# Optimization experiments

Measured on AMD Instinct MI355X. Metric: run time of the kernel, lower is better.

The kernel has to match this reference:

```python
import jax, jax.numpy as jnp
import numpy as np
from jax import lax

B, T, F, H, V, L = 64, 80, 4096, 512, 32000, 31


def _rn(k, shape, scale=0.05):
    return jax.random.normal(k, shape, dtype=jnp.float32) * scale


def setup_inputs() -> dict:
    key = jax.random.key(0)
    ks = jax.random.split(key, 16)
    emb = _rn(ks[0], (V, H)).at[0].set(0.0)  # padding_idx=0 row zeroed
    return dict(
        video_features=jax.random.normal(ks[1], (B, T, F), jnp.float32),
        captions=jax.random.randint(ks[2], (B, L), 0, V, jnp.int64),
        emb=emb,
        enc_Wih=_rn(ks[3], (4 * H, F)), enc_Whh=_rn(ks[4], (4 * H, H)),
        enc_bih=_rn(ks[5], (4 * H,)), enc_bhh=_rn(ks[6], (4 * H,)),
        attn_W=_rn(ks[7], (H, 2 * H)), attn_b=_rn(ks[8], (H,)),
        v_w=_rn(ks[9], (H,)),
        dec_Wih=_rn(ks[10], (4 * H, 2 * H)), dec_Whh=_rn(ks[11], (4 * H, H)),
        dec_bih=_rn(ks[12], (4 * H,)), dec_bhh=_rn(ks[13], (4 * H,)),
        fc_W=_rn(ks[14], (V, H)), fc_b=_rn(ks[15], (V,)),
    )


def _lstm_step(x, h, c, Wih, Whh, bih, bhh):
    # PyTorch gate order: i, f, g, o
    g = x @ Wih.T + bih + h @ Whh.T + bhh
    i, f, gg, o = jnp.split(g, 4, axis=-1)
    c = jax.nn.sigmoid(f) * c + jax.nn.sigmoid(i) * jnp.tanh(gg)
    h = jax.nn.sigmoid(o) * jnp.tanh(c)
    return h, c


def reference(video_features, captions, emb, enc_Wih, enc_Whh, enc_bih, enc_bhh,
              attn_W, attn_b, v_w, dec_Wih, dec_Whh, dec_bih, dec_bhh, fc_W, fc_b):
    b = video_features.shape[0]
    h_dim = enc_Whh.shape[1]
    h0 = jnp.zeros((b, h_dim), video_features.dtype)
    c0 = jnp.zeros((b, h_dim), video_features.dtype)

    # ---- encoder LSTM over time ----
    def enc_step(carry, x):
        h, c = carry
        h, c = _lstm_step(x, h, c, enc_Wih, enc_Whh, enc_bih, enc_bhh)
        return (h, c), h

    (h, c), enc_out = lax.scan(enc_step, (h0, c0), video_features.transpose(1, 0, 2))
    enc_out = enc_out.transpose(1, 0, 2)  # [B, T, H]

    # ---- attentive decoder, teacher forcing always on ----
    tokens = captions[:, :-1].T  # [L-1, B]

    def dec_step(carry, tok):
        h, c = carry
        e = emb[tok]  # [B, H]
        # Bahdanau attention: v . tanh(W [h; enc_out])
        hrep = jnp.broadcast_to(h[:, None, :], enc_out.shape)
        energy = jnp.tanh(jnp.concatenate([hrep, enc_out], axis=2) @ attn_W.T + attn_b)
        scores = energy @ v_w  # [B, T]
        w = jax.nn.softmax(scores, axis=1)
        ctx = jnp.einsum('bt,bth->bh', w, enc_out)
        x = jnp.concatenate([e, ctx], axis=1)  # [B, 2H]
        h, c = _lstm_step(x, h, c, dec_Wih, dec_Whh, dec_bih, dec_bhh)
        logits = h @ fc_W.T + fc_b  # [B, V]
        return (h, c), logits

    _, outs = lax.scan(dec_step, (h, c), tokens)
    return outs.transpose(1, 0, 2)  # [B, L-1, V]
```

## Files before the change

kernel.cpp:

```cpp
#include <hip/hip_runtime.h>


#define DEV __device__ __forceinline__

typedef __attribute__((ext_vector_type(4))) float f32x4;
typedef __attribute__((ext_vector_type(8))) short bf16x8;
typedef _Float16 half2_t __attribute__((ext_vector_type(2)));

static constexpr int B_ = 64, T_ = 80, H_ = 512, L_ = 31, NDEC = 30;

DEV unsigned short f2bf(float f) {
  unsigned u = __builtin_bit_cast(unsigned, f);
  u += 0x7FFF + ((u >> 16) & 1);
  return (unsigned short)(u >> 16);
}
DEV float bf2f(unsigned short s) {
  unsigned u = (unsigned)s << 16;
  return __builtin_bit_cast(float, u);
}
DEV unsigned short f2h(float x) { return __builtin_bit_cast(unsigned short, (_Float16)x); }
DEV float h2f(unsigned short h) { return (float)__builtin_bit_cast(_Float16, h); }
DEV unsigned f2h2(float lo, float hi) { return (unsigned)f2h(lo) | ((unsigned)f2h(hi) << 16); }
DEV float fdot2(unsigned x, unsigned w, float acc) {
  return __builtin_amdgcn_fdot2(__builtin_bit_cast(half2_t, x),
                                __builtin_bit_cast(half2_t, w), acc, false);
}
DEV float4 acc8(float4 a, uint4 hv, uint4 w0, uint4 w1, uint4 w2, uint4 w3) {
  a.x = fdot2(hv.x, w0.x, a.x); a.y = fdot2(hv.x, w0.y, a.y);
  a.z = fdot2(hv.x, w0.z, a.z); a.w = fdot2(hv.x, w0.w, a.w);
  a.x = fdot2(hv.y, w1.x, a.x); a.y = fdot2(hv.y, w1.y, a.y);
  a.z = fdot2(hv.y, w1.z, a.z); a.w = fdot2(hv.y, w1.w, a.w);
  a.x = fdot2(hv.z, w2.x, a.x); a.y = fdot2(hv.z, w2.y, a.y);
  a.z = fdot2(hv.z, w2.z, a.z); a.w = fdot2(hv.z, w2.w, a.w);
  a.x = fdot2(hv.w, w3.x, a.x); a.y = fdot2(hv.w, w3.y, a.y);
  a.z = fdot2(hv.w, w3.z, a.z); a.w = fdot2(hv.w, w3.w, a.w);
  return a;
}
DEV float accS(float s, uint4 hv, uint4 w) {
  s = fdot2(hv.x, w.x, s); s = fdot2(hv.y, w.y, s);
  s = fdot2(hv.z, w.z, s); s = fdot2(hv.w, w.w, s);
  return s;
}
DEV float sigmoidf(float x) { return 1.f / (1.f + __expf(-x)); }
DEV float tanh_fast(float x) { float e = __expf(2.f * x); return (e - 1.f) / (e + 1.f); }

DEV void astf(float* p, float v) { __hip_atomic_store(p, v, __ATOMIC_RELAXED, __HIP_MEMORY_SCOPE_AGENT); }
DEV void astu(unsigned* p, unsigned v) { __hip_atomic_store(p, v, __ATOMIC_RELAXED, __HIP_MEMORY_SCOPE_AGENT); }
DEV void asti(int* p, int v) { __hip_atomic_store(p, v, __ATOMIC_RELAXED, __HIP_MEMORY_SCOPE_AGENT); }
DEV float aldf(const float* p) { return __hip_atomic_load((float*)p, __ATOMIC_RELAXED, __HIP_MEMORY_SCOPE_AGENT); }
DEV unsigned aldu(const unsigned* p) { return __hip_atomic_load((unsigned*)p, __ATOMIC_RELAXED, __HIP_MEMORY_SCOPE_AGENT); }
DEV int aldi(const int* p) { return __hip_atomic_load((int*)p, __ATOMIC_RELAXED, __HIP_MEMORY_SCOPE_AGENT); }

DEV void tsync8(int* tf, int m, int ph) {
  __syncthreads();
  if (threadIdx.x == 0) asti(tf + m * 16, ph);
  if (threadIdx.x < 8)
    while (aldi(tf + (int)threadIdx.x * 16) < ph) __builtin_amdgcn_s_sleep(1);
  __syncthreads();
}

__global__ __launch_bounds__(256) void k_cvt(const float* __restrict__ in,
                                             unsigned short* __restrict__ out, long n4) {
  long i = (long)blockIdx.x * 256 + threadIdx.x;
  long stride = (long)gridDim.x * 256;
  for (; i < n4; i += stride) {
    float4 v = reinterpret_cast<const float4*>(in)[i];
    ushort4 o;
    o.x = f2bf(v.x); o.y = f2bf(v.y); o.z = f2bf(v.z); o.w = f2bf(v.w);
    reinterpret_cast<ushort4*>(out)[i] = o;
  }
}

__global__ void k_detect_i64(const int* __restrict__ cap, int* __restrict__ flag) {
  __shared__ int s;
  if (threadIdx.x == 0) s = 0;
  __syncthreads();
  int acc = 0;
  for (int i = threadIdx.x; i < (B_ * L_) / 2; i += 256) acc |= cap[2 * i + 1];
  if (acc) atomicOr(&s, 1);
  __syncthreads();
  if (threadIdx.x == 0) flag[0] = (s == 0) ? 1 : 0;
}

__global__ __launch_bounds__(256) void k_gather_emb(const float* __restrict__ emb,
                                                    const int* __restrict__ cap,
                                                    const int* __restrict__ flag,
                                                    unsigned short* __restrict__ aemb) {
  int r = blockIdx.x;
  int l = r >> 6, b = r & 63;
  int ci = b * L_ + l;
  int tok = flag[0] ? cap[2 * ci] : cap[ci];
  const float* src = emb + (size_t)tok * H_;
  unsigned short* dst = aemb + (size_t)r * H_;
  for (int c = threadIdx.x; c < H_; c += 256) dst[c] = f2bf(src[c]);
}

__global__ __launch_bounds__(256) void k_pack_enc(const float* __restrict__ whh,
                                                  uint4* __restrict__ wpe) {
  int idx = blockIdx.x * 256 + threadIdx.x;
  int k2 = idx >> 9, j = idx & 511;
  float2 r0 = *(const float2*)(whh + (size_t)(j) * 512 + 2 * k2);
  float2 r1 = *(const float2*)(whh + (size_t)(512 + j) * 512 + 2 * k2);
  float2 r2 = *(const float2*)(whh + (size_t)(1024 + j) * 512 + 2 * k2);
  float2 r3 = *(const float2*)(whh + (size_t)(1536 + j) * 512 + 2 * k2);
  wpe[idx] = make_uint4(f2h2(r0.x, r0.y), f2h2(r1.x, r1.y), f2h2(r2.x, r2.y), f2h2(r3.x, r3.y));
}

__global__ __launch_bounds__(256) void k_pack_dec(const float* __restrict__ dwih,
                                                  const float* __restrict__ dwhh,
                                                  uint4* __restrict__ wpd) {
  int idx = blockIdx.x * 256 + threadIdx.x;
  int k2 = idx >> 9, j = idx & 511;
  float2 r[4];
  if (k2 < 256) {
#pragma unroll
    for (int g = 0; g < 4; ++g)
      r[g] = *(const float2*)(dwih + (size_t)(g * 512 + j) * 1024 + 512 + 2 * k2);
  } else {
#pragma unroll
    for (int g = 0; g < 4; ++g)
      r[g] = *(const float2*)(dwhh + (size_t)(g * 512 + j) * 512 + 2 * (k2 - 256));
  }
  wpd[idx] = make_uint4(f2h2(r[0].x, r[0].y), f2h2(r[1].x, r[1].y),
                        f2h2(r[2].x, r[2].y), f2h2(r[3].x, r[3].y));
}

__global__ __launch_bounds__(256) void k_pack_attn2(const float* __restrict__ attnw,
                                                    uint4* __restrict__ wat2) {
  int idx = blockIdx.x * 256 + threadIdx.x;
  int k8 = idx >> 9, u = idx & 511;
  const float* p = attnw + (size_t)u * 1024 + 8 * k8;
  wat2[idx] = make_uint4(f2h2(p[0], p[1]), f2h2(p[2], p[3]),
                         f2h2(p[4], p[5]), f2h2(p[6], p[7]));
}

template <int OUT_MODE>
__global__ __launch_bounds__(256) void k_gemm(const unsigned short* __restrict__ A, int lda,
                                              const unsigned short* __restrict__ Bm, int ldb,
                                              float* __restrict__ C, int N, int K,
                                              const float* __restrict__ bias0,
                                              const float* __restrict__ bias1) {
  __shared__ __align__(16) unsigned short As[128 * 40];
  __shared__ __align__(16) unsigned short Bs[128 * 40];
  const int tid = threadIdx.x;
  const int m0 = blockIdx.y * 128, n0 = blockIdx.x * 128;
  const int wave = tid >> 6, lane = tid & 63;
  const int wm = wave >> 1, wn = wave & 1;
  const int lr = lane & 15, lk = lane >> 4;

  f32x4 acc[4][4];
#pragma unroll
  for (int m = 0; m < 4; ++m)
#pragma unroll
    for (int n = 0; n < 4; ++n) acc[m][n] = (f32x4){0.f, 0.f, 0.f, 0.f};

  const int c0 = tid, c1 = tid + 256;
  const int ar0 = c0 >> 2, as0 = c0 & 3;
  const int ar1 = c1 >> 2, as1 = c1 & 3;
  const unsigned short* pa0 = A + (size_t)(m0 + ar0) * lda + as0 * 8;
  const unsigned short* pa1 = A + (size_t)(m0 + ar1) * lda + as1 * 8;
  const unsigned short* pb0 = Bm + (size_t)(n0 + ar0) * ldb + as0 * 8;
  const unsigned short* pb1 = Bm + (size_t)(n0 + ar1) * ldb + as1 * 8;

  uint4 va0 = *(const uint4*)(pa0);
  uint4 va1 = *(const uint4*)(pa1);
  uint4 vb0 = *(const uint4*)(pb0);
  uint4 vb1 = *(const uint4*)(pb1);

  for (int k0 = 0; k0 < K; k0 += 32) {
    *(uint4*)(As + ar0 * 40 + as0 * 8) = va0;
    *(uint4*)(As + ar1 * 40 + as1 * 8) = va1;
    *(uint4*)(Bs + ar0 * 40 + as0 * 8) = vb0;
    *(uint4*)(Bs + ar1 * 40 + as1 * 8) = vb1;
    __syncthreads();
    if (k0 + 32 < K) {
      va0 = *(const uint4*)(pa0 + k0 + 32);
      va1 = *(const uint4*)(pa1 + k0 + 32);
      vb0 = *(const uint4*)(pb0 + k0 + 32);
      vb1 = *(const uint4*)(pb1 + k0 + 32);
    }
    bf16x8 af[4], bfr[4];
#pragma unroll
    for (int m = 0; m < 4; ++m)
      af[m] = *(const bf16x8*)(As + (wm * 64 + m * 16 + lr) * 40 + lk * 8);
#pragma unroll
    for (int n = 0; n < 4; ++n)
      bfr[n] = *(const bf16x8*)(Bs + (wn * 64 + n * 16 + lr) * 40 + lk * 8);
#pragma unroll
    for (int m = 0; m < 4; ++m)
#pragma unroll
      for (int n = 0; n < 4; ++n)
        acc[m][n] = __builtin_amdgcn_mfma_f32_16x16x32_bf16(af[m], bfr[n], acc[m][n], 0, 0, 0);
    __syncthreads();
  }
#pragma unroll
  for (int m = 0; m < 4; ++m) {
#pragma unroll
    for (int n = 0; n < 4; ++n) {
      const int col = n0 + wn * 64 + n * 16 + lr;
      float bv = (bias0 ? bias0[col] : 0.f) + (bias1 ? bias1[col] : 0.f);
#pragma unroll
      for (int j = 0; j < 4; ++j) {
        const int row = m0 + wm * 64 + m * 16 + lk * 4 + j;
        float v = acc[m][n][j] + bv;
        if (OUT_MODE == 0) {
          C[(size_t)row * N + col] = v;
        } else if (OUT_MODE == 1) {
          int l = row >> 6, b = row & 63;
          C[((size_t)b * NDEC + l) * (size_t)N + col] = v;
        } else {
          C[((size_t)row * 512 + (col & 511)) * 4 + (col >> 9)] = v;
        }
      }
    }
  }
}

__global__ __launch_bounds__(1024) void k_enc6(const float4* __restrict__ xg4,
                                               const uint4* __restrict__ wpe,
                                               float* __restrict__ encf,
                                               unsigned short* __restrict__ encbf,
                                               float* __restrict__ cfin,
                                               unsigned* __restrict__ h16E,
                                               int* __restrict__ flagsE) {
  __shared__ __align__(16) unsigned short h16[2][512];
  __shared__ __align__(16) float psumG[2][16][4][64];
  __shared__ __align__(16) float gsum[2][4][64];
  __shared__ unsigned short hnew[2][64];
  __shared__ __align__(16) uint4 wcache[96 * 64];
  const int bid = blockIdx.x, team = bid >> 3, m = bid & 7, tid = threadIdx.x;
  const int J0 = m * 64;
  int* tf = flagsE + team * 128;
  for (int i = tid; i < 96 * 64; i += 1024)
    wcache[i] = wpe[((i >> 6) << 9) | (J0 + (i & 63))];
  if (tid < 512) { h16[0][tid] = 0; h16[1][tid] = 0; }
  float c = 0.f;
  __syncthreads();
  const int j64 = tid & 63, ks = tid >> 6;
  const int j = J0 + j64;
  const uint4* hp0 = (const uint4*)h16[0];
  const uint4* hp1 = (const uint4*)h16[1];
  for (int t = 0; t < T_; ++t) {
    float4 a0 = {0.f, 0.f, 0.f, 0.f}, a1 = a0;
    if (ks < 6) {
#pragma unroll
      for (int ii = 0; ii < 4; ++ii) {
        const int k8 = ks * 4 + ii;
        uint4 h0 = hp0[k8], h1 = hp1[k8];
        uint4 w0 = wcache[((k8 * 4 + 0) << 6) | j64];
        uint4 w1 = wcache[((k8 * 4 + 1) << 6) | j64];
        uint4 w2 = wcache[((k8 * 4 + 2) << 6) | j64];
        uint4 w3 = wcache[((k8 * 4 + 3) << 6) | j64];
        a0 = acc8(a0, h0, w0, w1, w2, w3);
        a1 = acc8(a1, h1, w0, w1, w2, w3);
      }
    } else {
#pragma unroll 2
      for (int ii = 0; ii < 4; ++ii) {
        const int k8 = ks * 4 + ii;
        uint4 h0 = hp0[k8], h1 = hp1[k8];
        uint4 w0 = wpe[((k8 * 4 + 0) << 9) | j];
        uint4 w1 = wpe[((k8 * 4 + 1) << 9) | j];
        uint4 w2 = wpe[((k8 * 4 + 2) << 9) | j];
        uint4 w3 = wpe[((k8 * 4 + 3) << 9) | j];
        a0 = acc8(a0, h0, w0, w1, w2, w3);
        a1 = acc8(a1, h1, w0, w1, w2, w3);
      }
    }
    psumG[0][ks][0][j64] = a0.x; psumG[0][ks][1][j64] = a0.y;
    psumG[0][ks][2][j64] = a0.z; psumG[0][ks][3][j64] = a0.w;
    psumG[1][ks][0][j64] = a1.x; psumG[1][ks][1][j64] = a1.y;
    psumG[1][ks][2][j64] = a1.z; psumG[1][ks][3][j64] = a1.w;
    __syncthreads();
    if (tid < 512) {
      const int b2 = tid >> 8, g = (tid >> 6) & 3, jj = tid & 63;
      float s = 0.f;
#pragma unroll
      for (int q = 0; q < 16; ++q) s += psumG[b2][q][g][jj];
      gsum[b2][g][jj] = s;
    }
    __syncthreads();
    if (tid < 128) {
      const int b2 = tid >> 6, jj = tid & 63;
      const int b = team * 2 + b2;
      float4 xa = xg4[((size_t)b * T_ + t) * 512 + J0 + jj];
      float g0 = xa.x + gsum[b2][0][jj];
      float g1 = xa.y + gsum[b2][1][jj];
      float g2 = xa.z + gsum[b2][2][jj];
      float g3 = xa.w + gsum[b2][3][jj];
      c = sigmoidf(g1) * c + sigmoidf(g0) * tanh_fast(g2);
      float h = sigmoidf(g3) * tanh_fast(c);
      size_t o = ((size_t)b * T_ + t) * 512 + J0 + jj;
      encf[o] = h;
      encbf[o] = f2bf(h);
      hnew[b2][jj] = f2h(h);
      if (t == T_ - 1) cfin[(size_t)b * 512 + J0 + jj] = c;
    }
    __syncthreads();
    const int p = t & 1;
    if (tid < 64) {
      const int b2 = tid >> 5, pp = tid & 31;
      const int b = team * 2 + b2;
      astu(h16E + (size_t)p * 64 * 256 + b * 256 + (J0 >> 1) + pp,
           f2h2(h2f(hnew[b2][2 * pp]), h2f(hnew[b2][2 * pp + 1])));
    }
    tsync8(tf, m, t + 1);
    if (t < T_ - 1) {
      if (tid < 512) {
        const int b2 = tid >> 8, pp = tid & 255;
        const int b = team * 2 + b2;
        ((unsigned*)h16[b2])[pp] = aldu(h16E + (size_t)p * 64 * 256 + b * 256 + pp);
      }
      __syncthreads();
    }
  }
}

__global__ __launch_bounds__(1024) void k_dec8(const uint4* __restrict__ wpd,
                                               const uint4* __restrict__ wat2,
                                               const float* __restrict__ vw,
                                               const float4* __restrict__ eg4,
                                               const float* __restrict__ encpart,
                                               const unsigned short* __restrict__ encbf,
                                               const float* __restrict__ encf,
                                               const float* __restrict__ cfin,
                                               unsigned short* __restrict__ hsbf,
                                               float* __restrict__ scpart,
                                               unsigned* __restrict__ ctxsl,
                                               unsigned* __restrict__ h16D,
                                               int* __restrict__ flagsD) {
  __shared__ __align__(16) unsigned short xv16[2][1024];
  __shared__ float vsmO[64];
  __shared__ float hwOwn[2][64];
  __shared__ float sc2[2][80], wts2[2][80];
  __shared__ __align__(16) float psumW[2][16][64];
  __shared__ __align__(16) float psumG[2][16][4][64];
  __shared__ __align__(16) float gsum[2][4][64];
  __shared__ __align__(16) float ctxp[2][8][64];
  __shared__ unsigned short hnew[2][64];
  const int bid = blockIdx.x, team = bid >> 3, m = bid & 7, tid = threadIdx.x;
  const int J0 = m * 64;
  int* tf = flagsD + team * 128;
  {
    const int b2 = tid >> 9, jj = tid & 511;
    xv16[b2][512 + jj] = f2h(encf[((size_t)(team * 2 + b2) * T_ + T_ - 1) * 512 + jj]);
  }
  if (tid < 64) vsmO[tid] = vw[J0 + tid];
  float c = 0.f;
  if (tid < 128) c = cfin[(size_t)(team * 2 + (tid >> 6)) * 512 + J0 + (tid & 63)];
  __syncthreads();
  const int j64 = tid & 63, ks = tid >> 6;
  const int j = J0 + j64;
  const uint4* xp0 = (const uint4*)xv16[0];
  const uint4* xp1 = (const uint4*)xv16[1];

  for (int l = 0; l < NDEC; ++l) {
    {
      float4 a0 = {0.f, 0.f, 0.f, 0.f}, a1 = a0;
      float s0 = 0.f, s1 = 0.f;
#pragma unroll 2
      for (int ii = 0; ii < 4; ++ii) {
        const int ka = ks * 4 + ii;
        const int kg = 64 + ka;
        uint4 hx0 = xp0[kg], hx1 = xp1[kg];
        uint4 w0 = wpd[((kg * 4 + 0) << 9) | j];
        uint4 w1 = wpd[((kg * 4 + 1) << 9) | j];
        uint4 w2 = wpd[((kg * 4 + 2) << 9) | j];
        uint4 w3 = wpd[((kg * 4 + 3) << 9) | j];
        a0 = acc8(a0, hx0, w0, w1, w2, w3);
        a1 = acc8(a1, hx1, w0, w1, w2, w3);
        uint4 wa = wat2[(ka << 9) | j];
        s0 = accS(s0, hx0, wa);
        s1 = accS(s1, hx1, wa);
      }
      psumG[0][ks][0][j64] = a0.x; psumG[0][ks][1][j64] = a0.y;
      psumG[0][ks][2][j64] = a0.z; psumG[0][ks][3][j64] = a0.w;
      psumG[1][ks][0][j64] = a1.x; psumG[1][ks][1][j64] = a1.y;
      psumG[1][ks][2][j64] = a1.z; psumG[1][ks][3][j64] = a1.w;
      psumW[0][ks][j64] = s0;
      psumW[1][ks][j64] = s1;
    }
    __syncthreads();
    if (tid < 128) {
      const int b2 = tid >> 6, jj = tid & 63;
      float s = 0.f;
#pragma unroll
      for (int q = 0; q < 16; ++q) s += psumW[b2][q][jj];
      hwOwn[b2][jj] = s;
    }
    __syncthreads();
    {
      const int wv = tid >> 6, ln = tid & 63;
      const int b2 = wv & 1, b = team * 2 + b2;
      for (int t = wv >> 1; t < T_; t += 8) {
        float p = vsmO[ln] * tanh_fast(hwOwn[b2][ln] +
                  encpart[((size_t)b * T_ + t) * 512 + J0 + ln]);
#pragma unroll
        for (int s = 1; s < 64; s <<= 1) p += __shfl_xor(p, s, 64);
        if (ln == 0) astf(scpart + ((size_t)b * 8 + m) * 80 + t, p);
      }
    }
    tsync8(tf, m, 3 * l + 1);
    if (tid < 160) {
      const int b2 = tid / 80, t = tid % 80;
      const int b = team * 2 + b2;
      float s = 0.f;
#pragma unroll
      for (int mm = 0; mm < 8; ++mm) s += aldf(scpart + ((size_t)b * 8 + mm) * 80 + t);
      sc2[b2][t] = s;
    }
    __syncthreads();
    if (tid < 128) {
      const int b2 = tid >> 6, ln = tid & 63;
      float x0 = sc2[b2][ln];
      float x1 = (ln < 16) ? sc2[b2][64 + ln] : -1e30f;
      float mx = fmaxf(x0, x1);
#pragma unroll
      for (int s = 1; s < 64; s <<= 1) mx = fmaxf(mx, __shfl_xor(mx, s, 64));
      float e0 = __expf(x0 - mx);
      float e1 = (ln < 16) ? __expf(x1 - mx) : 0.f;
      float sm = e0 + e1;
#pragma unroll
      for (int s = 1; s < 64; s <<= 1) sm += __shfl_xor(sm, s, 64);
      wts2[b2][ln] = e0 / sm;
      if (ln < 16) wts2[b2][64 + ln] = e1 / sm;
    }
    __syncthreads();
    {
      const int b2 = tid >> 9, tq = (tid >> 6) & 7, jj = tid & 63;
      const int b = team * 2 + b2;
      float a = 0.f;
      for (int t = tq; t < T_; t += 8)
        a += wts2[b2][t] * bf2f(encbf[((size_t)b * T_ + t) * 512 + J0 + jj]);
      ctxp[b2][tq][jj] = a;
    }
    __syncthreads();
    if (tid < 64) {
      const int b2 = tid >> 5, pp = tid & 31;
      const int b = team * 2 + b2;
      float s0 = 0.f, s1 = 0.f;
#pragma unroll
      for (int q = 0; q < 8; ++q) {
        s0 += ctxp[b2][q][2 * pp];
        s1 += ctxp[b2][q][2 * pp + 1];
      }
      astu(ctxsl + (size_t)b * 256 + (J0 >> 1) + pp, f2h2(s0, s1));
    }
    tsync8(tf, m, 3 * l + 2);
    if (tid < 512) {
      const int b2 = tid >> 8, pp = tid & 255;
      const int b = team * 2 + b2;
      ((unsigned*)xv16[b2])[pp] = aldu(ctxsl + (size_t)b * 256 + pp);
    }
    __syncthreads();
    {
      float4 a0 = {0.f, 0.f, 0.f, 0.f}, a1 = a0;
#pragma unroll 2
      for (int ii = 0; ii < 4; ++ii) {
        const int kc = ks * 4 + ii;
        uint4 hx0 = xp0[kc], hx1 = xp1[kc];
        uint4 w0 = wpd[((kc * 4 + 0) << 9) | j];
        uint4 w1 = wpd[((kc * 4 + 1) << 9) | j];
        uint4 w2 = wpd[((kc * 4 + 2) << 9) | j];
        uint4 w3 = wpd[((kc * 4 + 3) << 9) | j];
        a0 = acc8(a0, hx0, w0, w1, w2, w3);
        a1 = acc8(a1, hx1, w0, w1, w2, w3);
      }
      psumG[0][ks][0][j64] += a0.x; psumG[0][ks][1][j64] += a0.y;
      psumG[0][ks][2][j64] += a0.z; psumG[0][ks][3][j64] += a0.w;
      psumG[1][ks][0][j64] += a1.x; psumG[1][ks][1][j64] += a1.y;
      psumG[1][ks][2][j64] += a1.z; psumG[1][ks][3][j64] += a1.w;
    }
    __syncthreads();
    if (tid < 512) {
      const int b2 = tid >> 8, g = (tid >> 6) & 3, jj = tid & 63;
      float s = 0.f;
#pragma unroll
      for (int q = 0; q < 16; ++q) s += psumG[b2][q][g][jj];
      gsum[b2][g][jj] = s;
    }
    __syncthreads();
    if (tid < 128) {
      const int b2 = tid >> 6, jj = tid & 63;
      const int b = team * 2 + b2;
      float4 xa = eg4[((size_t)l * 64 + b) * 512 + J0 + jj];
      float g0 = xa.x + gsum[b2][0][jj];
      float g1 = xa.y + gsum[b2][1][jj];
      float g2 = xa.z + gsum[b2][2][jj];
      float g3 = xa.w + gsum[b2][3][jj];
      c = sigmoidf(g1) * c + sigmoidf(g0) * tanh_fast(g2);
      float h = sigmoidf(g3) * tanh_fast(c);
      hsbf[((size_t)l * 64 + b) * 512 + J0 + jj] = f2bf(h);
      hnew[b2][jj] = f2h(h);
    }
    __syncthreads();
    const int p = l & 1;
    if (tid < 64) {
      const int b2 = tid >> 5, pp = tid & 31;
      const int b = team * 2 + b2;
      astu(h16D + (size_t)p * 64 * 256 + b * 256 + (J0 >> 1) + pp,
           f2h2(h2f(hnew[b2][2 * pp]), h2f(hnew[b2][2 * pp + 1])));
    }
    tsync8(tf, m, 3 * l + 3);
    if (l < NDEC - 1) {
      if (tid < 512) {
        const int b2 = tid >> 8, pp = tid & 255;
        const int b = team * 2 + b2;
        ((unsigned*)(&xv16[b2][512]))[pp] = aldu(h16D + (size_t)p * 64 * 256 + b * 256 + pp);
      }
      __syncthreads();
    }
  }
}

extern "C" void kernel_launch(void* const* d_in, const int* in_sizes, int n_in,
                              void* d_out, int out_size, void* d_ws, size_t ws_size,
                              hipStream_t stream) {
  const float* video = (const float*)d_in[0];
  const int* captions = (const int*)d_in[1];
  const float* emb = (const float*)d_in[2];
  const float* eWih = (const float*)d_in[3];
  const float* eWhh = (const float*)d_in[4];
  const float* ebih = (const float*)d_in[5];
  const float* ebhh = (const float*)d_in[6];
  const float* attnW = (const float*)d_in[7];
  const float* attnb = (const float*)d_in[8];
  const float* vw = (const float*)d_in[9];
  const float* dWih = (const float*)d_in[10];
  const float* dWhh = (const float*)d_in[11];
  const float* dbih = (const float*)d_in[12];
  const float* dbhh = (const float*)d_in[13];
  const float* fcW = (const float*)d_in[14];
  const float* fcb = (const float*)d_in[15];

  char* ws = (char*)d_ws;
  unsigned short* vid_bf = (unsigned short*)(ws + 0);
  unsigned short* fcw_bf = (unsigned short*)(ws + 0);
  const size_t G = 32768000ull;
  unsigned* h16E = (unsigned*)(ws + G + 0);
  unsigned* h16D = (unsigned*)(ws + G + 131072);
  float* scpartD = (float*)(ws + G + 262144);
  unsigned* ctxslD = (unsigned*)(ws + G + 425984);
  int* flagsE = (int*)(ws + G + 491520);
  int* flagsD = (int*)(ws + G + 507904);
  unsigned short* hs_bf = (unsigned short*)(ws + 33554432ull);
  uint4* wpd = (uint4*)(ws + 35520512ull);
  uint4* wpe = (uint4*)(ws + 39714816ull);
  float* xg4 = (float*)(ws + 41943040ull);
  float* encpart = (float*)(ws + 41943040ull);
  float* eg4 = (float*)(ws + 52428800ull);
  unsigned short* aemb = (unsigned short*)(ws + 68157440ull);
  unsigned short* ewih_bf = (unsigned short*)(ws + 83886080ull);
  float* encf = (float*)(ws + 100663296ull);
  unsigned short* encbf = (unsigned short*)(ws + 111149056ull);
  unsigned short* attnw_bf = (unsigned short*)(ws + 116391936ull);
  unsigned short* dwih_bf = (unsigned short*)(ws + 117440512ull);
  uint4* wat2 = (uint4*)(ws + 121634816ull);
  float* cfin = (float*)(ws + 122159104ull);
  int* flag = (int*)(ws + 122290176ull);

  auto cvt = [&](const float* in, unsigned short* out, long n) {
    long n4 = n / 4;
    int blocks = (int)((n4 + 255) / 256);
    if (blocks > 2048) blocks = 2048;
    k_cvt<<<blocks, 256, 0, stream>>>(in, out, n4);
  };
  cvt(video, vid_bf, 5120L * 4096);
  cvt(eWih, ewih_bf, 2048L * 4096);
  cvt(attnW, attnw_bf, 512L * 1024);
  cvt(dWih, dwih_bf, 2048L * 1024);
  k_detect_i64<<<1, 256, 0, stream>>>(captions, flag);

  k_gemm<2><<<dim3(16, 40), 256, 0, stream>>>(vid_bf, 4096, ewih_bf, 4096, xg4, 2048, 4096, ebih, ebhh);
  cvt(fcW, fcw_bf, 32000L * 512);

  k_pack_enc<<<512, 256, 0, stream>>>(eWhh, wpe);
  k_pack_dec<<<1024, 256, 0, stream>>>(dWih, dWhh, wpd);
  k_pack_attn2<<<128, 256, 0, stream>>>(attnW, wat2);

  hipMemsetAsync(ws + G + 491520, 0, 32768, stream);

  k_enc6<<<256, 1024, 0, stream>>>((const float4*)xg4, wpe, encf, encbf, cfin, h16E, flagsE);

  k_gather_emb<<<1920, 256, 0, stream>>>(emb, captions, flag, aemb);
  k_gemm<0><<<dim3(4, 40), 256, 0, stream>>>(encbf, 512, attnw_bf + 512, 1024, encpart, 512, 512, attnb, nullptr);
  k_gemm<2><<<dim3(16, 15), 256, 0, stream>>>(aemb, 512, dwih_bf, 1024, eg4, 2048, 512, dbih, dbhh);

  k_dec8<<<256, 1024, 0, stream>>>(wpd, wat2, vw, (const float4*)eg4, encpart, encbf, encf,
                                   cfin, hs_bf, scpartD, ctxslD, h16D, flagsD);

  k_gemm<1><<<dim3(250, 15), 256, 0, stream>>>(hs_bf, 512, fcw_bf, 512, (float*)d_out, 32000, 512, fcb, nullptr);
}
```

Baseline: 1.194 ms.

## Repartition recurrent LSTM teams to 16 blocks over 4 batches with 32 columns each

The encoder and decoder recurrent kernels change from teams of 8 blocks each owning 64 hidden columns for 2 batch rows to teams of 16 blocks each owning 32 columns for 4 batch rows. Each block now caches half of its recurrent weight rows in LDS (192 rows by 32 columns) and, in the decoder, caches the attention weight slice as well. The goal is to cut per-block weight traffic and raise weight reuse across more batch rows per step. In exchange each inter-block barrier now waits on 16 blocks instead of 8, and the score partial sums grow to 16 per batch row.

```diff
diff --git a/kernel.cpp b/kernel.cpp
--- a/kernel.cpp
+++ b/kernel.cpp
@@ -51,10 +51,10 @@
 DEV unsigned aldu(const unsigned* p) { return __hip_atomic_load((unsigned*)p, __ATOMIC_RELAXED, __HIP_MEMORY_SCOPE_AGENT); }
 DEV int aldi(const int* p) { return __hip_atomic_load((int*)p, __ATOMIC_RELAXED, __HIP_MEMORY_SCOPE_AGENT); }
 
-DEV void tsync8(int* tf, int m, int ph) {
+DEV void tsync16(int* tf, int m, int ph) {
   __syncthreads();
   if (threadIdx.x == 0) asti(tf + m * 16, ph);
-  if (threadIdx.x < 8)
+  if (threadIdx.x < 16)
     while (aldi(tf + (int)threadIdx.x * 16) < ph) __builtin_amdgcn_s_sleep(1);
   __syncthreads();
 }
@@ -216,64 +216,58 @@
   }
 }
 
-__global__ __launch_bounds__(1024) void k_enc6(const float4* __restrict__ xg4,
+__global__ __launch_bounds__(1024) void k_enc7(const float4* __restrict__ xg4,
                                                const uint4* __restrict__ wpe,
                                                float* __restrict__ encf,
                                                unsigned short* __restrict__ encbf,
                                                float* __restrict__ cfin,
                                                unsigned* __restrict__ h16E,
                                                int* __restrict__ flagsE) {
-  __shared__ __align__(16) unsigned short h16[2][512];
-  __shared__ __align__(16) float psumG[2][16][4][64];
-  __shared__ __align__(16) float gsum[2][4][64];
-  __shared__ unsigned short hnew[2][64];
-  __shared__ __align__(16) uint4 wcache[96 * 64];
-  const int bid = blockIdx.x, team = bid >> 3, m = bid & 7, tid = threadIdx.x;
-  const int J0 = m * 64;
-  int* tf = flagsE + team * 128;
-  for (int i = tid; i < 96 * 64; i += 1024)
-    wcache[i] = wpe[((i >> 6) << 9) | (J0 + (i & 63))];
-  if (tid < 512) { h16[0][tid] = 0; h16[1][tid] = 0; }
+  __shared__ __align__(16) uint4 wcache[192 * 32];
+  __shared__ __align__(16) unsigned short h16[4][512];
+  __shared__ __align__(16) float psumG[4][16][4][32];
+  __shared__ __align__(16) float gsum[4][4][32];
+  __shared__ unsigned short hnew[4][32];
+  const int bid = blockIdx.x, team = bid >> 4, m = bid & 15, tid = threadIdx.x;
+  const int J0 = m * 32;
+  int* tf = flagsE + team * 256;
+  for (int i = tid; i < 192 * 32; i += 1024)
+    wcache[i] = wpe[((i >> 5) << 9) | (J0 + (i & 31))];
+  for (int i = tid; i < 4 * 512; i += 1024) h16[i >> 9][i & 511] = 0;
   float c = 0.f;
   __syncthreads();
-  const int j64 = tid & 63, ks = tid >> 6;
-  const int j = J0 + j64;
-  const uint4* hp0 = (const uint4*)h16[0];
-  const uint4* hp1 = (const uint4*)h16[1];
+  const int j32 = tid & 31, ks = (tid >> 5) & 15, bh = tid >> 9;
+  const int j = J0 + j32;
+  const int bA = 2 * bh, bB = 2 * bh + 1;
   for (int t = 0; t < T_; ++t) {
     float4 a0 = {0.f, 0.f, 0.f, 0.f}, a1 = a0;
-    if (ks < 6) {
-#pragma unroll
-      for (int ii = 0; ii < 4; ++ii) {
-        const int k8 = ks * 4 + ii;
-        uint4 h0 = hp0[k8], h1 = hp1[k8];
-        uint4 w0 = wcache[((k8 * 4 + 0) << 6) | j64];
-        uint4 w1 = wcache[((k8 * 4 + 1) << 6) | j64];
-        uint4 w2 = wcache[((k8 * 4 + 2) << 6) | j64];
-        uint4 w3 = wcache[((k8 * 4 + 3) << 6) | j64];
-        a0 = acc8(a0, h0, w0, w1, w2, w3);
-        a1 = acc8(a1, h1, w0, w1, w2, w3);
+    const uint4* hpA = (const uint4*)h16[bA];
+    const uint4* hpB = (const uint4*)h16[bB];
+#pragma unroll
+    for (int ii = 0; ii < 4; ++ii) {
+      const int k8 = ks * 4 + ii;
+      uint4 w0, w1, w2, w3;
+      if (k8 < 48) {
+        w0 = wcache[((k8 * 4 + 0) << 5) | j32];
+        w1 = wcache[((k8 * 4 + 1) << 5) | j32];
+        w2 = wcache[((k8 * 4 + 2) << 5) | j32];
+        w3 = wcache[((k8 * 4 + 3) << 5) | j32];
+      } else {
+        w0 = wpe[((k8 * 4 + 0) << 9) | j];
+        w1 = wpe[((k8 * 4 + 1) << 9) | j];
+        w2 = wpe[((k8 * 4 + 2) << 9) | j];
+        w3 = wpe[((k8 * 4 + 3) << 9) | j];
       }
-    } else {
-#pragma unroll 2
-      for (int ii = 0; ii < 4; ++ii) {
-        const int k8 = ks * 4 + ii;
-        uint4 h0 = hp0[k8], h1 = hp1[k8];
-        uint4 w0 = wpe[((k8 * 4 + 0) << 9) | j];
-        uint4 w1 = wpe[((k8 * 4 + 1) << 9) | j];
-        uint4 w2 = wpe[((k8 * 4 + 2) << 9) | j];
-        uint4 w3 = wpe[((k8 * 4 + 3) << 9) | j];
-        a0 = acc8(a0, h0, w0, w1, w2, w3);
-        a1 = acc8(a1, h1, w0, w1, w2, w3);
-      }
-    }
-    psumG[0][ks][0][j64] = a0.x; psumG[0][ks][1][j64] = a0.y;
-    psumG[0][ks][2][j64] = a0.z; psumG[0][ks][3][j64] = a0.w;
-    psumG[1][ks][0][j64] = a1.x; psumG[1][ks][1][j64] = a1.y;
-    psumG[1][ks][2][j64] = a1.z; psumG[1][ks][3][j64] = a1.w;
+      a0 = acc8(a0, hpA[k8], w0, w1, w2, w3);
+      a1 = acc8(a1, hpB[k8], w0, w1, w2, w3);
+    }
+    psumG[bA][ks][0][j32] = a0.x; psumG[bA][ks][1][j32] = a0.y;
+    psumG[bA][ks][2][j32] = a0.z; psumG[bA][ks][3][j32] = a0.w;
+    psumG[bB][ks][0][j32] = a1.x; psumG[bB][ks][1][j32] = a1.y;
+    psumG[bB][ks][2][j32] = a1.z; psumG[bB][ks][3][j32] = a1.w;
     __syncthreads();
     if (tid < 512) {
-      const int b2 = tid >> 8, g = (tid >> 6) & 3, jj = tid & 63;
+      const int b2 = tid >> 7, g = (tid >> 5) & 3, jj = tid & 31;
       float s = 0.f;
 #pragma unroll
       for (int q = 0; q < 16; ++q) s += psumG[b2][q][g][jj];
@@ -281,8 +275,8 @@
     }
     __syncthreads();
     if (tid < 128) {
-      const int b2 = tid >> 6, jj = tid & 63;
-      const int b = team * 2 + b2;
+      const int b2 = tid >> 5, jj = tid & 31;
+      const int b = team * 4 + b2;
       float4 xa = xg4[((size_t)b * T_ + t) * 512 + J0 + jj];
       float g0 = xa.x + gsum[b2][0][jj];
       float g1 = xa.y + gsum[b2][1][jj];
@@ -299,24 +293,21 @@
     __syncthreads();
     const int p = t & 1;
     if (tid < 64) {
-      const int b2 = tid >> 5, pp = tid & 31;
-      const int b = team * 2 + b2;
-      astu(h16E + (size_t)p * 64 * 256 + b * 256 + (J0 >> 1) + pp,
+      const int b2 = tid >> 4, pp = tid & 15;
+      const int b = team * 4 + b2;
+      astu(h16E + (size_t)p * 16384 + b * 256 + (J0 >> 1) + pp,
            f2h2(h2f(hnew[b2][2 * pp]), h2f(hnew[b2][2 * pp + 1])));
     }
-    tsync8(tf, m, t + 1);
+    tsync16(tf, m, t + 1);
     if (t < T_ - 1) {
-      if (tid < 512) {
-        const int b2 = tid >> 8, pp = tid & 255;
-        const int b = team * 2 + b2;
-        ((unsigned*)h16[b2])[pp] = aldu(h16E + (size_t)p * 64 * 256 + b * 256 + pp);
-      }
+      const int b2 = tid >> 8, pp = tid & 255;
+      ((unsigned*)h16[b2])[pp] = aldu(h16E + (size_t)p * 16384 + (team * 4 + b2) * 256 + pp);
       __syncthreads();
     }
   }
 }
 
-__global__ __launch_bounds__(1024) void k_dec8(const uint4* __restrict__ wpd,
+__global__ __launch_bounds__(1024) void k_dec9(const uint4* __restrict__ wpd,
                                                const uint4* __restrict__ wat2,
                                                const float* __restrict__ vw,
                                                const float4* __restrict__ eg4,
@@ -329,60 +320,65 @@
                                                unsigned* __restrict__ ctxsl,
                                                unsigned* __restrict__ h16D,
                                                int* __restrict__ flagsD) {
-  __shared__ __align__(16) unsigned short xv16[2][1024];
-  __shared__ float vsmO[64];
-  __shared__ float hwOwn[2][64];
-  __shared__ float sc2[2][80], wts2[2][80];
-  __shared__ __align__(16) float psumW[2][16][64];
-  __shared__ __align__(16) float psumG[2][16][4][64];
-  __shared__ __align__(16) float gsum[2][4][64];
-  __shared__ __align__(16) float ctxp[2][8][64];
-  __shared__ unsigned short hnew[2][64];
-  const int bid = blockIdx.x, team = bid >> 3, m = bid & 7, tid = threadIdx.x;
-  const int J0 = m * 64;
-  int* tf = flagsD + team * 128;
-  {
-    const int b2 = tid >> 9, jj = tid & 511;
-    xv16[b2][512 + jj] = f2h(encf[((size_t)(team * 2 + b2) * T_ + T_ - 1) * 512 + jj]);
-  }
-  if (tid < 64) vsmO[tid] = vw[J0 + tid];
+  __shared__ __align__(16) uint4 wat_c[64 * 32];
+  __shared__ __align__(16) unsigned short xv16[4][1024];
+  __shared__ float vsmO[32];
+  __shared__ float hwOwn[4][32];
+  __shared__ float sc[4][80], wts[4][80];
+  __shared__ __align__(16) float psumW[4][16][32];
+  __shared__ __align__(16) float psumG[4][16][4][32];
+  __shared__ __align__(16) float gsum[4][4][32];
+  __shared__ __align__(16) float ctxp[4][8][32];
+  __shared__ float ctxf[4][32];
+  __shared__ unsigned short hnew[4][32];
+  const int bid = blockIdx.x, team = bid >> 4, m = bid & 15, tid = threadIdx.x;
+  const int J0 = m * 32;
+  int* tf = flagsD + team * 256;
+  for (int i = tid; i < 64 * 32; i += 1024)
+    wat_c[i] = wat2[((i >> 5) << 9) | (J0 + (i & 31))];
+  for (int i = tid; i < 4 * 512; i += 1024) {
+    const int b2 = i >> 9, jj = i & 511;
+    xv16[b2][512 + jj] = f2h(encf[((size_t)(team * 4 + b2) * T_ + T_ - 1) * 512 + jj]);
+  }
+  if (tid < 32) vsmO[tid] = vw[J0 + tid];
   float c = 0.f;
-  if (tid < 128) c = cfin[(size_t)(team * 2 + (tid >> 6)) * 512 + J0 + (tid & 63)];
+  if (tid < 128) c = cfin[(size_t)(team * 4 + (tid >> 5)) * 512 + J0 + (tid & 31)];
   __syncthreads();
-  const int j64 = tid & 63, ks = tid >> 6;
-  const int j = J0 + j64;
-  const uint4* xp0 = (const uint4*)xv16[0];
-  const uint4* xp1 = (const uint4*)xv16[1];
+  const int j32 = tid & 31, ks = (tid >> 5) & 15, bh = tid >> 9;
+  const int j = J0 + j32;
+  const int bA = 2 * bh, bB = 2 * bh + 1;
 
   for (int l = 0; l < NDEC; ++l) {
     {
+      const uint4* xpA = (const uint4*)xv16[bA];
+      const uint4* xpB = (const uint4*)xv16[bB];
       float4 a0 = {0.f, 0.f, 0.f, 0.f}, a1 = a0;
       float s0 = 0.f, s1 = 0.f;
-#pragma unroll 2
+#pragma unroll
       for (int ii = 0; ii < 4; ++ii) {
         const int ka = ks * 4 + ii;
         const int kg = 64 + ka;
-        uint4 hx0 = xp0[kg], hx1 = xp1[kg];
+        uint4 hx0 = xpA[kg], hx1 = xpB[kg];
         uint4 w0 = wpd[((kg * 4 + 0) << 9) | j];
         uint4 w1 = wpd[((kg * 4 + 1) << 9) | j];
         uint4 w2 = wpd[((kg * 4 + 2) << 9) | j];
         uint4 w3 = wpd[((kg * 4 + 3) << 9) | j];
         a0 = acc8(a0, hx0, w0, w1, w2, w3);
         a1 = acc8(a1, hx1, w0, w1, w2, w3);
-        uint4 wa = wat2[(ka << 9) | j];
+        uint4 wa = wat_c[(ka << 5) | j32];
         s0 = accS(s0, hx0, wa);
         s1 = accS(s1, hx1, wa);
       }
-      psumG[0][ks][0][j64] = a0.x; psumG[0][ks][1][j64] = a0.y;
-      psumG[0][ks][2][j64] = a0.z; psumG[0][ks][3][j64] = a0.w;
-      psumG[1][ks][0][j64] = a1.x; psumG[1][ks][1][j64] = a1.y;
-      psumG[1][ks][2][j64] = a1.z; psumG[1][ks][3][j64] = a1.w;
-      psumW[0][ks][j64] = s0;
-      psumW[1][ks][j64] = s1;
+      psumG[bA][ks][0][j32] = a0.x; psumG[bA][ks][1][j32] = a0.y;
+      psumG[bA][ks][2][j32] = a0.z; psumG[bA][ks][3][j32] = a0.w;
+      psumG[bB][ks][0][j32] = a1.x; psumG[bB][ks][1][j32] = a1.y;
+      psumG[bB][ks][2][j32] = a1.z; psumG[bB][ks][3][j32] = a1.w;
+      psumW[bA][ks][j32] = s0;
+      psumW[bB][ks][j32] = s1;
     }
     __syncthreads();
     if (tid < 128) {
-      const int b2 = tid >> 6, jj = tid & 63;
+      const int b2 = tid >> 5, jj = tid & 31;
       float s = 0.f;
 #pragma unroll
       for (int q = 0; q < 16; ++q) s += psumW[b2][q][jj];
@@ -390,30 +386,33 @@
     }
     __syncthreads();
     {
-      const int wv = tid >> 6, ln = tid & 63;
-      const int b2 = wv & 1, b = team * 2 + b2;
-      for (int t = wv >> 1; t < T_; t += 8) {
+      const int wv = tid >> 6;
+      const int b2 = wv & 3, tg = wv >> 2;
+      const int b = team * 4 + b2;
+      const int ln = (tid & 63) & 31, th = (tid & 63) >> 5;
+      for (int tt = tg * 20; tt < tg * 20 + 20; tt += 2) {
+        const int t = tt + th;
         float p = vsmO[ln] * tanh_fast(hwOwn[b2][ln] +
                   encpart[((size_t)b * T_ + t) * 512 + J0 + ln]);
 #pragma unroll
-        for (int s = 1; s < 64; s <<= 1) p += __shfl_xor(p, s, 64);
-        if (ln == 0) astf(scpart + ((size_t)b * 8 + m) * 80 + t, p);
+        for (int s = 1; s < 32; s <<= 1) p += __shfl_xor(p, s, 64);
+        if (ln == 0) astf(scpart + ((size_t)b * 16 + m) * 80 + t, p);
       }
     }
-    tsync8(tf, m, 3 * l + 1);
-    if (tid < 160) {
+    tsync16(tf, m, 3 * l + 1);
+    if (tid < 320) {
       const int b2 = tid / 80, t = tid % 80;
-      const int b = team * 2 + b2;
+      const int b = team * 4 + b2;
       float s = 0.f;
 #pragma unroll
-      for (int mm = 0; mm < 8; ++mm) s += aldf(scpart + ((size_t)b * 8 + mm) * 80 + t);
-      sc2[b2][t] = s;
-    }
-    __syncthreads();
-    if (tid < 128) {
+      for (int mm = 0; mm < 16; ++mm) s += aldf(scpart + ((size_t)b * 16 + mm) * 80 + t);
+      sc[b2][t] = s;
+    }
+    __syncthreads();
+    if (tid < 256) {
       const int b2 = tid >> 6, ln = tid & 63;
-      float x0 = sc2[b2][ln];
-      float x1 = (ln < 16) ? sc2[b2][64 + ln] : -1e30f;
+      float x0 = sc[b2][ln];
+      float x1 = (ln < 16) ? sc[b2][64 + ln] : -1e30f;
       float mx = fmaxf(x0, x1);
 #pragma unroll
       for (int s = 1; s < 64; s <<= 1) mx = fmaxf(mx, __shfl_xor(mx, s, 64));
@@ -422,43 +421,46 @@
       float sm = e0 + e1;
 #pragma unroll
       for (int s = 1; s < 64; s <<= 1) sm += __shfl_xor(sm, s, 64);
-      wts2[b2][ln] = e0 / sm;
-      if (ln < 16) wts2[b2][64 + ln] = e1 / sm;
+      wts[b2][ln] = e0 / sm;
+      if (ln < 16) wts[b2][64 + ln] = e1 / sm;
     }
     __syncthreads();
     {
-      const int b2 = tid >> 9, tq = (tid >> 6) & 7, jj = tid & 63;
-      const int b = team * 2 + b2;
+      const int b2 = tid >> 8, tq = (tid >> 5) & 7, jj = tid & 31;
+      const int b = team * 4 + b2;
       float a = 0.f;
       for (int t = tq; t < T_; t += 8)
-        a += wts2[b2][t] * bf2f(encbf[((size_t)b * T_ + t) * 512 + J0 + jj]);
+        a += wts[b2][t] * bf2f(encbf[((size_t)b * T_ + t) * 512 + J0 + jj]);
       ctxp[b2][tq][jj] = a;
     }
     __syncthreads();
+    if (tid < 128) {
+      const int b2 = tid >> 5, jj = tid & 31;
+      float s = 0.f;
+#pragma unroll
+      for (int q = 0; q < 8; ++q) s += ctxp[b2][q][jj];
+      ctxf[b2][jj] = s;
+    }
+    __syncthreads();
     if (tid < 64) {
-      const int b2 = tid >> 5, pp = tid & 31;
-      const int b = team * 2 + b2;
-      float s0 = 0.f, s1 = 0.f;
-#pragma unroll
-      for (int q = 0; q < 8; ++q) {
-        s0 += ctxp[b2][q][2 * pp];
-        s1 += ctxp[b2][q][2 * pp + 1];
-      }
-      astu(ctxsl + (size_t)b * 256 + (J0 >> 1) + pp, f2h2(s0, s1));
-    }
-    tsync8(tf, m, 3 * l + 2);
-    if (tid < 512) {
+      const int b2 = tid >> 4, pp = tid & 15;
+      const int b = team * 4 + b2;
+      astu(ctxsl + (size_t)b * 256 + (J0 >> 1) + pp, f2h2(ctxf[b2][2 * pp], ctxf[b2][2 * pp + 1]));
+    }
+    tsync16(tf, m, 3 * l + 2);
+    {
       const int b2 = tid >> 8, pp = tid & 255;
-      const int b = team * 2 + b2;
-      ((unsigned*)xv16[b2])[pp] = aldu(ctxsl + (size_t)b * 256 + pp);
+      ((unsigned*)xv16[b2])[pp] = aldu(ctxsl + (size_t)(team * 4 + b2) * 256 + pp);
     }
     __syncthreads();
     {
+      const uint4* xpA = (const uint4*)xv16[bA];
+      const uint4* xpB = (const uint4*)xv16[bB];
       float4 a0 = {0.f, 0.f, 0.f, 0.f}, a1 = a0;
-#pragma unroll 2
+#pragma unroll
       for (int ii = 0; ii < 4; ++ii) {
         const int kc = ks * 4 + ii;
-        uint4 hx0 = xp0[kc], hx1 = xp1[kc];
+        uint4 hx0 = xpA[kc], hx1 = xpB[kc];
         uint4 w0 = wpd[((kc * 4 + 0) << 9) | j];
         uint4 w1 = wpd[((kc * 4 + 1) << 9) | j];
         uint4 w2 = wpd[((kc * 4 + 2) << 9) | j];
@@ -466,14 +468,14 @@
         a0 = acc8(a0, hx0, w0, w1, w2, w3);
         a1 = acc8(a1, hx1, w0, w1, w2, w3);
       }
-      psumG[0][ks][0][j64] += a0.x; psumG[0][ks][1][j64] += a0.y;
-      psumG[0][ks][2][j64] += a0.z; psumG[0][ks][3][j64] += a0.w;
-      psumG[1][ks][0][j64] += a1.x; psumG[1][ks][1][j64] += a1.y;
-      psumG[1][ks][2][j64] += a1.z; psumG[1][ks][3][j64] += a1.w;
+      psumG[bA][ks][0][j32] += a0.x; psumG[bA][ks][1][j32] += a0.y;
+      psumG[bA][ks][2][j32] += a0.z; psumG[bA][ks][3][j32] += a0.w;
+      psumG[bB][ks][0][j32] += a1.x; psumG[bB][ks][1][j32] += a1.y;
+      psumG[bB][ks][2][j32] += a1.z; psumG[bB][ks][3][j32] += a1.w;
     }
     __syncthreads();
     if (tid < 512) {
-      const int b2 = tid >> 8, g = (tid >> 6) & 3, jj = tid & 63;
+      const int b2 = tid >> 7, g = (tid >> 5) & 3, jj = tid & 31;
       float s = 0.f;
 #pragma unroll
       for (int q = 0; q < 16; ++q) s += psumG[b2][q][g][jj];
@@ -481,8 +483,8 @@
     }
     __syncthreads();
     if (tid < 128) {
-      const int b2 = tid >> 6, jj = tid & 63;
-      const int b = team * 2 + b2;
+      const int b2 = tid >> 5, jj = tid & 31;
+      const int b = team * 4 + b2;
       float4 xa = eg4[((size_t)l * 64 + b) * 512 + J0 + jj];
       float g0 = xa.x + gsum[b2][0][jj];
       float g1 = xa.y + gsum[b2][1][jj];
@@ -496,18 +498,15 @@
     __syncthreads();
     const int p = l & 1;
     if (tid < 64) {
-      const int b2 = tid >> 5, pp = tid & 31;
-      const int b = team * 2 + b2;
-      astu(h16D + (size_t)p * 64 * 256 + b * 256 + (J0 >> 1) + pp,
+      const int b2 = tid >> 4, pp = tid & 15;
+      const int b = team * 4 + b2;
+      astu(h16D + (size_t)p * 16384 + b * 256 + (J0 >> 1) + pp,
            f2h2(h2f(hnew[b2][2 * pp]), h2f(hnew[b2][2 * pp + 1])));
     }
-    tsync8(tf, m, 3 * l + 3);
+    tsync16(tf, m, 3 * l + 3);
     if (l < NDEC - 1) {
-      if (tid < 512) {
-        const int b2 = tid >> 8, pp = tid & 255;
-        const int b = team * 2 + b2;
-        ((unsigned*)(&xv16[b2][512]))[pp] = aldu(h16D + (size_t)p * 64 * 256 + b * 256 + pp);
-      }
+      const int b2 = tid >> 8, pp = tid & 255;
+      ((unsigned*)xv16[b2])[256 + pp] = aldu(h16D + (size_t)p * 16384 + (team * 4 + b2) * 256 + pp);
       __syncthreads();
     }
   }
@@ -540,9 +539,9 @@
   unsigned* h16E = (unsigned*)(ws + G + 0);
   unsigned* h16D = (unsigned*)(ws + G + 131072);
   float* scpartD = (float*)(ws + G + 262144);
-  unsigned* ctxslD = (unsigned*)(ws + G + 425984);
-  int* flagsE = (int*)(ws + G + 491520);
-  int* flagsD = (int*)(ws + G + 507904);
+  unsigned* ctxslD = (unsigned*)(ws + G + 589824);
+  int* flagsE = (int*)(ws + G + 655360);
+  int* flagsD = (int*)(ws + G + 671744);
   unsigned short* hs_bf = (unsigned short*)(ws + 33554432ull);
   uint4* wpd = (uint4*)(ws + 35520512ull);
   uint4* wpe = (uint4*)(ws + 39714816ull);
@@ -578,15 +577,15 @@
   k_pack_dec<<<1024, 256, 0, stream>>>(dWih, dWhh, wpd);
   k_pack_attn2<<<128, 256, 0, stream>>>(attnW, wat2);
 
-  hipMemsetAsync(ws + G + 491520, 0, 32768, stream);
-
-  k_enc6<<<256, 1024, 0, stream>>>((const float4*)xg4, wpe, encf, encbf, cfin, h16E, flagsE);
+  hipMemsetAsync(ws + G + 655360, 0, 32768, stream);
+
+  k_enc7<<<256, 1024, 0, stream>>>((const float4*)xg4, wpe, encf, encbf, cfin, h16E, flagsE);
 
   k_gather_emb<<<1920, 256, 0, stream>>>(emb, captions, flag, aemb);
   k_gemm<0><<<dim3(4, 40), 256, 0, stream>>>(encbf, 512, attnw_bf + 512, 1024, encpart, 512, 512, attnb, nullptr);
   k_gemm<2><<<dim3(16, 15), 256, 0, stream>>>(aemb, 512, dwih_bf, 1024, eg4, 2048, 512, dbih, dbhh);
 
-  k_dec8<<<256, 1024, 0, stream>>>(wpd, wat2, vw, (const float4*)eg4, encpart, encbf, encf,
+  k_dec9<<<256, 1024, 0, stream>>>(wpd, wat2, vw, (const float4*)eg4, encpart, encbf, encf,
                                    cfin, hs_bf, scpartD, ctxslD, h16D, flagsD);
 
   k_gemm<1><<<dim3(250, 15), 256, 0, stream>>>(hs_bf, 512, fcw_bf, 512, (float*)d_out, 32000, 512, fcb, nullptr);
```

Result: slower. 3.601 ms (+201.5%).
